# Kernel optimization log

Hardware: AMD Instinct MI355X
Metric: run time of the kernel (lower is better)

## Reference

```python
import jax, jax.numpy as jnp
import numpy as np

N_NODES = 50000
N_EDGES = 800000
HID = 256
TDIM = 128


def setup_inputs() -> dict:
    key = jax.random.key(0)
    ks = jax.random.split(key, 16)
    s = 1.0 / np.sqrt(HID)
    inp = {
        "hidden": jax.random.normal(ks[0], (N_NODES, HID), dtype=jnp.float32),
        "t": jax.random.uniform(ks[1], (1,), dtype=jnp.float32) * 100.0,
        "src": jax.random.randint(ks[2], (N_EDGES,), 0, N_NODES, dtype=jnp.int32),
        "dst": jax.random.randint(ks[3], (N_EDGES,), 0, N_NODES, dtype=jnp.int32),
        # GraphConv layer 1 (relu) and layer 2 weights: [in, out]
        "W1": jax.random.normal(ks[4], (HID, HID), dtype=jnp.float32) * s,
        "b1": jnp.zeros((HID,), dtype=jnp.float32),
        "W2": jax.random.normal(ks[5], (HID, HID), dtype=jnp.float32) * s,
        "b2": jnp.zeros((HID,), dtype=jnp.float32),
        # TimeEncode: cos(t * w + b)
        "time_w": jnp.asarray(1.0 / 10.0 ** np.linspace(0, 9, TDIM), dtype=jnp.float32),
        "time_b": jnp.zeros((TDIM,), dtype=jnp.float32),
        # GRUCell params (torch layout: [3*H, in], gate order r,z,n)
        "W_ih": jax.random.normal(ks[6], (3 * HID, HID + TDIM), dtype=jnp.float32) * s,
        "W_hh": jax.random.normal(ks[7], (3 * HID, HID), dtype=jnp.float32) * s,
        "b_ih": jnp.zeros((3 * HID,), dtype=jnp.float32),
        "b_hh": jnp.zeros((3 * HID,), dtype=jnp.float32),
    }
    return inp


def _gcn_layer(x, W, b, src, dst, out_norm, in_norm, relu):
    # DGL GraphConv, norm='both', in==out feats -> aggregate then matmul
    h = x * out_norm[:, None]
    agg = jax.ops.segment_sum(h[src], dst, num_segments=N_NODES)
    agg = agg * in_norm[:, None]
    out = agg @ W + b
    return jax.nn.relu(out) if relu else out


def reference(hidden, t, src, dst, W1, b1, W2, b2, time_w, time_b, W_ih, W_hh, b_ih, b_hh):
    ones = jnp.ones((N_EDGES,), dtype=hidden.dtype)
    outdeg = jax.ops.segment_sum(ones, src, num_segments=N_NODES)
    indeg = jax.ops.segment_sum(ones, dst, num_segments=N_NODES)
    out_norm = jnp.clip(outdeg, 1.0, None) ** -0.5
    in_norm = jnp.clip(indeg, 1.0, None) ** -0.5

    # StackedGCN: k_hop-1 relu layers + final layer (no activation)
    h = _gcn_layer(hidden, W1, b1, src, dst, out_norm, in_norm, relu=True)
    h = _gcn_layer(h, W2, b2, src, dst, out_norm, in_norm, relu=False)
    h = jax.nn.relu(h)

    # time encoding: cos(t * w + b), broadcast to all nodes
    te = jnp.cos(t[0] * time_w + time_b)  # [TDIM]
    te = jnp.broadcast_to(te, (h.shape[0], TDIM))

    x = jnp.concatenate([h, te], axis=1)  # [N, HID+TDIM]

    # GRUCell (torch semantics)
    gi = x @ W_ih.T + b_ih
    gh = h @ W_hh.T + b_hh
    i_r, i_z, i_n = jnp.split(gi, 3, axis=1)
    h_r, h_z, h_n = jnp.split(gh, 3, axis=1)
    r = jax.nn.sigmoid(i_r + h_r)
    z = jax.nn.sigmoid(i_z + h_z)
    n = jnp.tanh(i_n + r * h_n)
    return (1.0 - z) * n + z * h
```

## Files before the change

### kernel.cpp

```cpp
#include <hip/hip_runtime.h>
#include <cstdint>
#include <cstddef>

#define NN 50000
#define NE 800000
#define HID 256
#define TDIM 128

#define CHB 16384
#define NSL 64
#define SLE (NE / NSL)

typedef short bf16x8 __attribute__((ext_vector_type(8)));
typedef float f32x4 __attribute__((ext_vector_type(4)));

#define GLOAD_LDS16(g, l)                                                        \
  __builtin_amdgcn_global_load_lds(                                              \
      (const __attribute__((address_space(1))) unsigned int*)(g),                \
      (__attribute__((address_space(3))) unsigned int*)(l), 16, 0, 0)

__device__ inline unsigned short f2bf(float f) {
  uint32_t u = __builtin_bit_cast(uint32_t, f);
  uint32_t r = u + 0x7FFFu + ((u >> 16) & 1u);
  return (unsigned short)(r >> 16);
}
__device__ inline float bf2f(unsigned short s) {
  uint32_t u = ((uint32_t)s) << 16;
  return __builtin_bit_cast(float, u);
}
__device__ inline float fast_sig(float x) {
  return __builtin_amdgcn_rcpf(1.0f + __expf(-x));
}
__device__ inline float fast_tanh(float x) {
  float xc = fminf(fmaxf(x, -10.0f), 10.0f);
  float e = __expf(2.0f * xc);
  return 1.0f - 2.0f * __builtin_amdgcn_rcpf(e + 1.0f);
}

__global__ __launch_bounds__(1024) void prep_a(const int* __restrict__ src,
                                               const int* __restrict__ dst,
                                               int* __restrict__ P,
                                               const float* __restrict__ x,
                                               short* __restrict__ xb,
                                               unsigned char* __restrict__ xf8) {
  const int b = blockIdx.x;
  if (b < 8 * NSL) {
    __shared__ int h[CHB];
    const int c = b & 7, s = b >> 3;
    for (int j = threadIdx.x; j < CHB; j += 1024) h[j] = 0;
    __syncthreads();
    const int* arr = (c < 4) ? src : dst;
    const int base = (c & 3) * CHB;
    const int e0 = s * SLE;
    for (int i = threadIdx.x; i < SLE; i += 1024) {
      int v = arr[e0 + i] - base;
      if ((unsigned)v < CHB) atomicAdd(&h[v], 1);
    }
    __syncthreads();
    int* Pc = P + (size_t)(c * NSL + s) * CHB;
    for (int j = threadIdx.x; j < CHB; j += 1024) Pc[j] = h[j];
  } else {
    int i = (b - 8 * NSL) * 1024 + threadIdx.x;
    if (i < NN * HID / 4) {
      float4 v = ((const float4*)x)[i];
      unsigned int lo = (unsigned int)f2bf(v.x) | ((unsigned int)f2bf(v.y) << 16);
      unsigned int hi = (unsigned int)f2bf(v.z) | ((unsigned int)f2bf(v.w) << 16);
      ((uint2*)xb)[i] = make_uint2(lo, hi);
      unsigned int f8 = __builtin_amdgcn_cvt_pk_fp8_f32(v.x, v.y, 0u, false);
      f8 = __builtin_amdgcn_cvt_pk_fp8_f32(v.z, v.w, f8, true);
      ((unsigned int*)xf8)[i] = f8;
    }
  }
}

__global__ __launch_bounds__(256) void hist_reduce(int* __restrict__ P,
                                                   float* __restrict__ onorm,
                                                   float* __restrict__ inorm,
                                                   int* __restrict__ icnt) {
  int n = blockIdx.x * 256 + threadIdx.x;
  if (n >= 4 * CHB) return;
  const int c = n >> 14, j = n & (CHB - 1);
  int* Po = P + (size_t)(c * NSL) * CHB + j;
  int od = 0;
#pragma unroll 8
  for (int s = 0; s < NSL; ++s) od += Po[(size_t)s * CHB];
  int* Pi = P + (size_t)((4 + c) * NSL) * CHB + j;
  int run = 0;
#pragma unroll 8
  for (int s = 0; s < NSL; ++s) { int t = Pi[(size_t)s * CHB]; Pi[(size_t)s * CHB] = run; run += t; }
  if (n < NN) {
    onorm[n] = 1.0f / sqrtf(fmaxf((float)od, 1.0f));
    inorm[n] = 1.0f / sqrtf(fmaxf((float)run, 1.0f));
    icnt[n] = run;
  }
}

__global__ __launch_bounds__(1024) void scan_rows(const int* __restrict__ icnt,
                                                  int* __restrict__ rowstart) {
  __shared__ int wsum[16];
  __shared__ int carry_s;
  const int tid = threadIdx.x, lane = tid & 63, w = tid >> 6;
  if (tid == 0) { carry_s = 0; rowstart[0] = 0; }
  __syncthreads();
  for (int base = 0; base < NN; base += 8192) {
    int i0 = base + tid * 8;
    int c[8];
    int v = 0;
#pragma unroll
    for (int j = 0; j < 8; ++j) {
      int i = i0 + j;
      c[j] = (i < NN) ? icnt[i] : 0;
      v += c[j];
    }
    int inc = v;
#pragma unroll
    for (int off = 1; off < 64; off <<= 1) {
      int t = __shfl_up(inc, off, 64);
      if (lane >= off) inc += t;
    }
    if (lane == 63) wsum[w] = inc;
    __syncthreads();
    int woff = 0;
    for (int k = 0; k < w; ++k) woff += wsum[k];
    int carry = carry_s;
    int run = carry + woff + inc - v;
#pragma unroll
    for (int j = 0; j < 8; ++j) {
      int i = i0 + j;
      if (i < NN) rowstart[i + 1] = run + c[j];
      run += c[j];
    }
    __syncthreads();
    if (tid == 1023) carry_s = carry + woff + inc;
    __syncthreads();
  }
}

__global__ __launch_bounds__(1024) void fill_csr2(const int* __restrict__ src,
                                                  const int* __restrict__ dst,
                                                  const float* __restrict__ onorm,
                                                  const int* __restrict__ rowstart,
                                                  const int* __restrict__ P,
                                                  uint2* __restrict__ epk) {
  __shared__ int cur[CHB];
  const int b = blockIdx.x;
  const int c = b & 3, s = b >> 2;
  const int base = c * CHB;
  const int* Pi = P + (size_t)((4 + c) * NSL + s) * CHB;
  for (int j = threadIdx.x; j < CHB; j += 1024) {
    int n = base + j;
    cur[j] = (n < NN ? rowstart[n] : 0) + Pi[j];
  }
  __syncthreads();
  const int e0 = s * SLE;
  for (int i = threadIdx.x; i < SLE; i += 1024) {
    int d = dst[e0 + i] - base;
    if ((unsigned)d < CHB) {
      int sv = src[e0 + i];
      int pos = atomicAdd(&cur[d], 1);
      epk[pos] = make_uint2((unsigned)sv, __builtin_bit_cast(unsigned, onorm[sv]));
    }
  }
}

__global__ __launch_bounds__(256) void gather_agg(const unsigned char* __restrict__ xF8,
                                                  const int* __restrict__ rowstart,
                                                  const uint2* __restrict__ epk,
                                                  const float* __restrict__ inorm,
                                                  short* __restrict__ aggB) {
  const int wid = blockIdx.x * 4 + (threadIdx.x >> 6);
  const int l = threadIdx.x & 63;
  if (wid >= NN) return;
  const int half = l >> 5;
  const int fo2 = (l & 31) * 8;
  const int e1 = rowstart[wid + 1];
  int e = rowstart[wid];
  float a[8] = {0.f, 0.f, 0.f, 0.f, 0.f, 0.f, 0.f, 0.f};

  for (; e + 8 <= e1; e += 8) {
    uint2 pe[4]; uint2 uu[4];
#pragma unroll
    for (int q = 0; q < 4; ++q) pe[q] = epk[e + q * 2 + half];
#pragma unroll
    for (int q = 0; q < 4; ++q) uu[q] = *(const uint2*)(xF8 + (size_t)pe[q].x * HID + fo2);
#pragma unroll
    for (int q = 0; q < 4; ++q) {
      float wq = __builtin_bit_cast(float, pe[q].y);
      a[0] = fmaf(__builtin_amdgcn_cvt_f32_fp8(uu[q].x, 0), wq, a[0]);
      a[1] = fmaf(__builtin_amdgcn_cvt_f32_fp8(uu[q].x, 1), wq, a[1]);
      a[2] = fmaf(__builtin_amdgcn_cvt_f32_fp8(uu[q].x, 2), wq, a[2]);
      a[3] = fmaf(__builtin_amdgcn_cvt_f32_fp8(uu[q].x, 3), wq, a[3]);
      a[4] = fmaf(__builtin_amdgcn_cvt_f32_fp8(uu[q].y, 0), wq, a[4]);
      a[5] = fmaf(__builtin_amdgcn_cvt_f32_fp8(uu[q].y, 1), wq, a[5]);
      a[6] = fmaf(__builtin_amdgcn_cvt_f32_fp8(uu[q].y, 2), wq, a[6]);
      a[7] = fmaf(__builtin_amdgcn_cvt_f32_fp8(uu[q].y, 3), wq, a[7]);
    }
  }
  for (; e < e1; e += 2) {
    int idx = e + half;
    bool v = idx < e1;
    uint2 pe = v ? epk[idx] : make_uint2(0u, 0u);
    float w0 = v ? __builtin_bit_cast(float, pe.y) : 0.0f;
    uint2 u = *(const uint2*)(xF8 + (size_t)pe.x * HID + fo2);
    a[0] = fmaf(__builtin_amdgcn_cvt_f32_fp8(u.x, 0), w0, a[0]);
    a[1] = fmaf(__builtin_amdgcn_cvt_f32_fp8(u.x, 1), w0, a[1]);
    a[2] = fmaf(__builtin_amdgcn_cvt_f32_fp8(u.x, 2), w0, a[2]);
    a[3] = fmaf(__builtin_amdgcn_cvt_f32_fp8(u.x, 3), w0, a[3]);
    a[4] = fmaf(__builtin_amdgcn_cvt_f32_fp8(u.y, 0), w0, a[4]);
    a[5] = fmaf(__builtin_amdgcn_cvt_f32_fp8(u.y, 1), w0, a[5]);
    a[6] = fmaf(__builtin_amdgcn_cvt_f32_fp8(u.y, 2), w0, a[6]);
    a[7] = fmaf(__builtin_amdgcn_cvt_f32_fp8(u.y, 3), w0, a[7]);
  }

#pragma unroll
  for (int k = 0; k < 8; ++k) a[k] += __shfl_xor(a[k], 32);

  if (l < 32) {
    const float wi = inorm[wid];
    uint4 o;
    o.x = (unsigned int)f2bf(a[0] * wi) | ((unsigned int)f2bf(a[1] * wi) << 16);
    o.y = (unsigned int)f2bf(a[2] * wi) | ((unsigned int)f2bf(a[3] * wi) << 16);
    o.z = (unsigned int)f2bf(a[4] * wi) | ((unsigned int)f2bf(a[5] * wi) << 16);
    o.w = (unsigned int)f2bf(a[6] * wi) | ((unsigned int)f2bf(a[7] * wi) << 16);
    *(uint4*)(aggB + (size_t)wid * HID + fo2) = o;
  }
}

__global__ __launch_bounds__(256) void wprep(const float* __restrict__ W1,
                                             const float* __restrict__ W2,
                                             const float* __restrict__ W_ih,
                                             const float* __restrict__ W_hh,
                                             const float* __restrict__ t,
                                             const float* __restrict__ tw,
                                             const float* __restrict__ tb,
                                             const float* __restrict__ b_ih,
                                             const float* __restrict__ b_hh,
                                             short* __restrict__ W1B,
                                             short* __restrict__ W2B,
                                             short* __restrict__ WgB,
                                             float* __restrict__ cst) {
  const int b = blockIdx.x;
  const int k = threadIdx.x;
  if (b < 256) {
    W1B[b * 256 + k] = (short)f2bf(W1[k * 256 + b]);
    W2B[b * 256 + k] = (short)f2bf(W2[k * 256 + b]);
  } else if (b < 512) {
    int u = b - 256;
    int base = (u >> 4) * 64 + (u & 15);
    float v0 = W_ih[(size_t)u * 384 + k] + W_hh[(size_t)u * 256 + k];
    float v1 = W_ih[(size_t)(256 + u) * 384 + k] + W_hh[(size_t)(256 + u) * 256 + k];
    float v2 = W_ih[(size_t)(512 + u) * 384 + k];
    float v3 = W_hh[(size_t)(512 + u) * 256 + k];
    WgB[(size_t)(base + 0)  * 256 + k] = (short)f2bf(v0);
    WgB[(size_t)(base + 16) * 256 + k] = (short)f2bf(v1);
    WgB[(size_t)(base + 32) * 256 + k] = (short)f2bf(v2);
    WgB[(size_t)(base + 48) * 256 + k] = (short)f2bf(v3);
  } else {
    __shared__ float te[TDIM];
    int u = k;
    if (u < TDIM) te[u] = cosf(t[0] * tw[u] + tb[u]);
    __syncthreads();
    float cr = b_ih[u] + b_hh[u];
    float cz = b_ih[256 + u] + b_hh[256 + u];
    float ci = b_ih[512 + u];
    for (int kk = 0; kk < TDIM; ++kk) {
      float tk = te[kk];
      cr = fmaf(tk, W_ih[(size_t)u * 384 + 256 + kk], cr);
      cz = fmaf(tk, W_ih[(size_t)(256 + u) * 384 + 256 + kk], cz);
      ci = fmaf(tk, W_ih[(size_t)(512 + u) * 384 + 256 + kk], ci);
    }
    cst[u] = cr;
    cst[256 + u] = cz;
    cst[512 + u] = ci;
    cst[768 + u] = b_hh[512 + u];
  }
}

template <int NP, bool GRUE, bool F8OUT>
__global__ __launch_bounds__(256, 3) void panel_gemm(const short* __restrict__ A,
                                                     const short* __restrict__ WB,
                                                     const float* __restrict__ bias,
                                                     const float* __restrict__ cst,
                                                     short* __restrict__ outH,
                                                     unsigned char* __restrict__ outF8,
                                                     float* __restrict__ outF) {
  __shared__ __align__(16) short Ps[64 * 256];

  const int row0 = blockIdx.x * 64;
  const int tid = threadIdx.x;
  const int l = tid & 63, w = tid >> 6;
  const int fr = l & 15, fg = l >> 4;

#pragma unroll
  for (int i = 0; i < 8; ++i) {
    int id = tid + i * 256;
    int row = id >> 5, kc = id & 31;
    GLOAD_LDS16(WB + (size_t)row * HID + ((kc ^ (row & 15)) << 3), Ps + id * 8);
  }

  int ar = row0 + w * 16 + fr;
  ar = ar < NN ? ar : NN - 1;
  bf16x8 af[8];
#pragma unroll
  for (int t = 0; t < 8; ++t)
    af[t] = *(const bf16x8*)(A + (size_t)ar * HID + t * 32 + fg * 8);

  __syncthreads();

#pragma unroll
  for (int p = 0; p < NP; ++p) {
    f32x4 acc[4];
    acc[0] = acc[1] = acc[2] = acc[3] = (f32x4)(0.0f);
#pragma unroll
    for (int t = 0; t < 8; ++t) {
#pragma unroll
      for (int nf = 0; nf < 4; ++nf) {
        int rr = nf * 16 + fr;
        bf16x8 bh = *(const bf16x8*)(Ps + rr * 256 + (((t * 4 + fg) ^ (rr & 15)) << 3));
        acc[nf] = __builtin_amdgcn_mfma_f32_16x16x32_bf16(af[t], bh, acc[nf], 0, 0, 0);
      }
    }

    if constexpr (!GRUE) {
#pragma unroll
      for (int nf = 0; nf < 4; ++nf) {
        int c = p * 64 + nf * 16 + fr;
        float bs = bias[c];
#pragma unroll
        for (int j = 0; j < 4; ++j) {
          int row = row0 + w * 16 + fg * 4 + j;
          if (row < NN) {
            float v = fmaxf(acc[nf][j] + bs, 0.0f);
            size_t off = (size_t)row * HID + c;
            outH[off] = (short)f2bf(v);
            if constexpr (F8OUT) {
              unsigned int r8 = __builtin_amdgcn_cvt_pk_fp8_f32(v, v, 0u, false);
              outF8[off] = (unsigned char)(r8 & 0xFF);
            }
          }
        }
      }
    } else {
      const int u = p * 16 + fr;
      const float cr = cst[u], cz = cst[256 + u], ci = cst[512 + u], chn = cst[768 + u];
#pragma unroll
      for (int j = 0; j < 4; ++j) {
        int row = row0 + w * 16 + fg * 4 + j;
        if (row < NN) {
          float dr = acc[0][j] + cr;
          float dz = acc[1][j] + cz;
          float dn = acc[2][j] + ci;
          float dh = acc[3][j] + chn;
          float rg = fast_sig(dr);
          float zg = fast_sig(dz);
          float ng = fast_tanh(dn + rg * dh);
          size_t off = (size_t)row * HID + u;
          float hv = bf2f((unsigned short)A[off]);
          outF[off] = (1.0f - zg) * ng + zg * hv;
        }
      }
    }

    if (p + 1 < NP) {
      __syncthreads();
#pragma unroll
      for (int i = 0; i < 8; ++i) {
        int id = tid + i * 256;
        int row = id >> 5, kc = id & 31;
        GLOAD_LDS16(WB + (size_t)((p + 1) * 64 + row) * HID + ((kc ^ (row & 15)) << 3),
                    Ps + id * 8);
      }
      __syncthreads();
    }
  }
}

extern "C" void kernel_launch(void* const* d_in, const int* in_sizes, int n_in,
                              void* d_out, int out_size, void* d_ws, size_t ws_size,
                              hipStream_t stream) {
  const float* hidden = (const float*)d_in[0];
  const float* t      = (const float*)d_in[1];
  const int*   src    = (const int*)d_in[2];
  const int*   dst    = (const int*)d_in[3];
  const float* W1     = (const float*)d_in[4];
  const float* b1     = (const float*)d_in[5];
  const float* W2     = (const float*)d_in[6];
  const float* b2     = (const float*)d_in[7];
  const float* time_w = (const float*)d_in[8];
  const float* time_b = (const float*)d_in[9];
  const float* W_ih   = (const float*)d_in[10];
  const float* W_hh   = (const float*)d_in[11];
  const float* b_ih   = (const float*)d_in[12];
  const float* b_hh   = (const float*)d_in[13];
  float* out = (float*)d_out;

  char* p = (char*)d_ws;
  float* onorm = (float*)p;      p += 50048 * 4;
  float* inorm = (float*)p;      p += 50048 * 4;
  float* cst   = (float*)p;      p += 1024 * 4;
  int* rowstart = (int*)p;       p += 50052 * 4;
  int* icnt     = (int*)p;       p += 50048 * 4;
  uint2* epk    = (uint2*)p;     p += 800000 * 8;
  const size_t NFE = (size_t)NN * HID;
  short* Xb   = (short*)p;       p += NFE * 2;
  short* aggB = (short*)p;       p += NFE * 2;
  short* h1B  = (short*)p;       p += NFE * 2;
  short* h2B  = (short*)p;       p += NFE * 2;
  unsigned char* Xf8  = (unsigned char*)p;  p += NFE;
  unsigned char* h1F8 = (unsigned char*)p;  p += NFE;
  short* W1B  = (short*)p;       p += 65536 * 2;
  short* W2B  = (short*)p;       p += 65536 * 2;
  short* WgB  = (short*)p;       p += 262144 * 2;
  int* P = (int*)h1B;

  const int cvt_blocks = (NN * HID / 4 + 1023) / 1024;
  prep_a<<<8 * NSL + cvt_blocks, 1024, 0, stream>>>(src, dst, P, hidden, Xb, Xf8);
  wprep<<<513, 256, 0, stream>>>(W1, W2, W_ih, W_hh, t, time_w, time_b, b_ih, b_hh,
                                 W1B, W2B, WgB, cst);

  hist_reduce<<<(4 * CHB + 255) / 256, 256, 0, stream>>>(P, onorm, inorm, icnt);
  scan_rows<<<1, 1024, 0, stream>>>(icnt, rowstart);
  fill_csr2<<<4 * NSL, 1024, 0, stream>>>(src, dst, onorm, rowstart, P, epk);

  const int gather_blocks = (NN + 3) / 4;
  const int gblocks = (NN + 63) / 64;

  gather_agg<<<gather_blocks, 256, 0, stream>>>(Xf8, rowstart, epk, inorm, aggB);
  panel_gemm<4, false, true><<<gblocks, 256, 0, stream>>>(aggB, W1B, b1, nullptr, h1B, h1F8, nullptr);

  gather_agg<<<gather_blocks, 256, 0, stream>>>(h1F8, rowstart, epk, inorm, aggB);
  panel_gemm<4, false, false><<<gblocks, 256, 0, stream>>>(aggB, W2B, b2, nullptr, h2B, nullptr, nullptr);

  panel_gemm<16, true, false><<<gblocks, 256, 0, stream>>>(h2B, WgB, nullptr, cst, nullptr, nullptr, out);
}
```

Measured before the change: 271.4 us.

## Fuse layer-2 GEMM with GRU GEMM via LDS-resident h2 tile

```diff
diff --git a/kernel.cpp b/kernel.cpp
--- a/kernel.cpp
+++ b/kernel.cpp
@@ -276,14 +276,11 @@
   }
 }
 
-template <int NP, bool GRUE, bool F8OUT>
+template <int NP>
 __global__ __launch_bounds__(256, 3) void panel_gemm(const short* __restrict__ A,
                                                      const short* __restrict__ WB,
                                                      const float* __restrict__ bias,
-                                                     const float* __restrict__ cst,
-                                                     short* __restrict__ outH,
-                                                     unsigned char* __restrict__ outF8,
-                                                     float* __restrict__ outF) {
+                                                     unsigned char* __restrict__ outF8) {
   __shared__ __align__(16) short Ps[64 * 256];
 
   const int row0 = blockIdx.x * 64;
@@ -321,42 +318,17 @@
       }
     }
 
-    if constexpr (!GRUE) {
-#pragma unroll
-      for (int nf = 0; nf < 4; ++nf) {
-        int c = p * 64 + nf * 16 + fr;
-        float bs = bias[c];
-#pragma unroll
-        for (int j = 0; j < 4; ++j) {
-          int row = row0 + w * 16 + fg * 4 + j;
-          if (row < NN) {
-            float v = fmaxf(acc[nf][j] + bs, 0.0f);
-            size_t off = (size_t)row * HID + c;
-            outH[off] = (short)f2bf(v);
-            if constexpr (F8OUT) {
-              unsigned int r8 = __builtin_amdgcn_cvt_pk_fp8_f32(v, v, 0u, false);
-              outF8[off] = (unsigned char)(r8 & 0xFF);
-            }
-          }
-        }
-      }
-    } else {
-      const int u = p * 16 + fr;
-      const float cr = cst[u], cz = cst[256 + u], ci = cst[512 + u], chn = cst[768 + u];
+#pragma unroll
+    for (int nf = 0; nf < 4; ++nf) {
+      int c = p * 64 + nf * 16 + fr;
+      float bs = bias[c];
 #pragma unroll
       for (int j = 0; j < 4; ++j) {
         int row = row0 + w * 16 + fg * 4 + j;
         if (row < NN) {
-          float dr = acc[0][j] + cr;
-          float dz = acc[1][j] + cz;
-          float dn = acc[2][j] + ci;
-          float dh = acc[3][j] + chn;
-          float rg = fast_sig(dr);
-          float zg = fast_sig(dz);
-          float ng = fast_tanh(dn + rg * dh);
-          size_t off = (size_t)row * HID + u;
-          float hv = bf2f((unsigned short)A[off]);
-          outF[off] = (1.0f - zg) * ng + zg * hv;
+          float v = fmaxf(acc[nf][j] + bs, 0.0f);
+          unsigned int r8 = __builtin_amdgcn_cvt_pk_fp8_f32(v, v, 0u, false);
+          outF8[(size_t)row * HID + c] = (unsigned char)(r8 & 0xFF);
         }
       }
     }
@@ -368,6 +340,133 @@
         int id = tid + i * 256;
         int row = id >> 5, kc = id & 31;
         GLOAD_LDS16(WB + (size_t)((p + 1) * 64 + row) * HID + ((kc ^ (row & 15)) << 3),
+                    Ps + id * 8);
+      }
+      __syncthreads();
+    }
+  }
+}
+
+__global__ __launch_bounds__(256, 2) void fused_l2gru(const short* __restrict__ A,
+                                                      const short* __restrict__ W2B,
+                                                      const float* __restrict__ b2,
+                                                      const short* __restrict__ WgB,
+                                                      const float* __restrict__ cst,
+                                                      float* __restrict__ outF) {
+  __shared__ __align__(16) short h2s[64 * 256];
+  __shared__ __align__(16) short Ps[64 * 256];
+
+  const int row0 = blockIdx.x * 64;
+  const int tid = threadIdx.x;
+  const int l = tid & 63, w = tid >> 6;
+  const int fr = l & 15, fg = l >> 4;
+
+#pragma unroll
+  for (int i = 0; i < 8; ++i) {
+    int id = tid + i * 256;
+    int row = id >> 5, kc = id & 31;
+    GLOAD_LDS16(W2B + (size_t)row * HID + ((kc ^ (row & 15)) << 3), Ps + id * 8);
+  }
+
+  int ar = row0 + w * 16 + fr;
+  ar = ar < NN ? ar : NN - 1;
+  bf16x8 af[8];
+#pragma unroll
+  for (int t = 0; t < 8; ++t)
+    af[t] = *(const bf16x8*)(A + (size_t)ar * HID + t * 32 + fg * 8);
+
+  __syncthreads();
+
+#pragma unroll
+  for (int ct = 0; ct < 4; ++ct) {
+    f32x4 acc[4];
+    acc[0] = acc[1] = acc[2] = acc[3] = (f32x4)(0.0f);
+#pragma unroll
+    for (int t = 0; t < 8; ++t) {
+#pragma unroll
+      for (int nf = 0; nf < 4; ++nf) {
+        int rr = nf * 16 + fr;
+        bf16x8 bh = *(const bf16x8*)(Ps + rr * 256 + (((t * 4 + fg) ^ (rr & 15)) << 3));
+        acc[nf] = __builtin_amdgcn_mfma_f32_16x16x32_bf16(af[t], bh, acc[nf], 0, 0, 0);
+      }
+    }
+#pragma unroll
+    for (int nf = 0; nf < 4; ++nf) {
+      int c = ct * 64 + nf * 16 + fr;
+      float bs = b2[c];
+#pragma unroll
+      for (int j = 0; j < 4; ++j) {
+        int lrow = w * 16 + fg * 4 + j;
+        float v = fmaxf(acc[nf][j] + bs, 0.0f);
+        h2s[lrow * 256 + ((((c >> 3) ^ (lrow & 15)) << 3) | (c & 7))] = (short)f2bf(v);
+      }
+    }
+    if (ct < 3) {
+      __syncthreads();
+#pragma unroll
+      for (int i = 0; i < 8; ++i) {
+        int id = tid + i * 256;
+        int row = id >> 5, kc = id & 31;
+        GLOAD_LDS16(W2B + (size_t)((ct + 1) * 64 + row) * HID + ((kc ^ (row & 15)) << 3),
+                    Ps + id * 8);
+      }
+      __syncthreads();
+    }
+  }
+
+  __syncthreads();
+
+  const int r2 = w * 16 + fr;
+  bf16x8 af2[8];
+#pragma unroll
+  for (int t = 0; t < 8; ++t)
+    af2[t] = *(const bf16x8*)(&h2s[r2 * 256 + (((t * 4 + fg) ^ fr) << 3)]);
+
+#pragma unroll
+  for (int i = 0; i < 8; ++i) {
+    int id = tid + i * 256;
+    int row = id >> 5, kc = id & 31;
+    GLOAD_LDS16(WgB + (size_t)row * HID + ((kc ^ (row & 15)) << 3), Ps + id * 8);
+  }
+  __syncthreads();
+
+  for (int cg = 0; cg < 16; ++cg) {
+    f32x4 acc[4];
+    acc[0] = acc[1] = acc[2] = acc[3] = (f32x4)(0.0f);
+#pragma unroll
+    for (int t = 0; t < 8; ++t) {
+#pragma unroll
+      for (int nf = 0; nf < 4; ++nf) {
+        int rr = nf * 16 + fr;
+        bf16x8 bh = *(const bf16x8*)(Ps + rr * 256 + (((t * 4 + fg) ^ (rr & 15)) << 3));
+        acc[nf] = __builtin_amdgcn_mfma_f32_16x16x32_bf16(af2[t], bh, acc[nf], 0, 0, 0);
+      }
+    }
+    const int u = cg * 16 + fr;
+    const float cr = cst[u], cz = cst[256 + u], ci = cst[512 + u], chn = cst[768 + u];
+#pragma unroll
+    for (int j = 0; j < 4; ++j) {
+      int lrow = w * 16 + fg * 4 + j;
+      int grow = row0 + lrow;
+      if (grow < NN) {
+        float dr = acc[0][j] + cr;
+        float dz = acc[1][j] + cz;
+        float dn = acc[2][j] + ci;
+        float dh = acc[3][j] + chn;
+        float rg = fast_sig(dr);
+        float zg = fast_sig(dz);
+        float ng = fast_tanh(dn + rg * dh);
+        float hv = bf2f((unsigned short)h2s[lrow * 256 + ((((u >> 3) ^ (lrow & 15)) << 3) | (u & 7))]);
+        outF[(size_t)grow * HID + u] = (1.0f - zg) * ng + zg * hv;
+      }
+    }
+    if (cg < 15) {
+      __syncthreads();
+#pragma unroll
+      for (int i = 0; i < 8; ++i) {
+        int id = tid + i * 256;
+        int row = id >> 5, kc = id & 31;
+        GLOAD_LDS16(WgB + (size_t)((cg + 1) * 64 + row) * HID + ((kc ^ (row & 15)) << 3),
                     Ps + id * 8);
       }
       __syncthreads();
@@ -404,14 +503,15 @@
   const size_t NFE = (size_t)NN * HID;
   short* Xb   = (short*)p;       p += NFE * 2;
   short* aggB = (short*)p;       p += NFE * 2;
-  short* h1B  = (short*)p;       p += NFE * 2;
-  short* h2B  = (short*)p;       p += NFE * 2;
+  char* scrA  = p;               p += NFE * 2;
+  char* scrB  = p;               p += NFE * 2;
   unsigned char* Xf8  = (unsigned char*)p;  p += NFE;
   unsigned char* h1F8 = (unsigned char*)p;  p += NFE;
   short* W1B  = (short*)p;       p += 65536 * 2;
   short* W2B  = (short*)p;       p += 65536 * 2;
   short* WgB  = (short*)p;       p += 262144 * 2;
-  int* P = (int*)h1B;
+  int* P = (int*)scrA;
+  (void)scrB;
 
   const int cvt_blocks = (NN * HID / 4 + 1023) / 1024;
   prep_a<<<8 * NSL + cvt_blocks, 1024, 0, stream>>>(src, dst, P, hidden, Xb, Xf8);
@@ -426,10 +526,8 @@
   const int gblocks = (NN + 63) / 64;
 
   gather_agg<<<gather_blocks, 256, 0, stream>>>(Xf8, rowstart, epk, inorm, aggB);
-  panel_gemm<4, false, true><<<gblocks, 256, 0, stream>>>(aggB, W1B, b1, nullptr, h1B, h1F8, nullptr);
+  panel_gemm<4><<<gblocks, 256, 0, stream>>>(aggB, W1B, b1, h1F8);
 
   gather_agg<<<gather_blocks, 256, 0, stream>>>(h1F8, rowstart, epk, inorm, aggB);
-  panel_gemm<4, false, false><<<gblocks, 256, 0, stream>>>(aggB, W2B, b2, nullptr, h2B, nullptr, nullptr);
-
-  panel_gemm<16, true, false><<<gblocks, 256, 0, stream>>>(h2B, WgB, nullptr, cst, nullptr, nullptr, out);
-}
+  fused_l2gru<<<gblocks, 256, 0, stream>>>(aggB, W2B, b2, WgB, cst, out);
+}
```

Result: slower. 276.9 us (+2.0%).
